# Kernel tuning notes

Measured on AMD Instinct MI355X. Metric: run time of the kernel, lower is better.

Reference implementation:

```python
import jax, jax.numpy as jnp
import numpy as np

B, T, K = 2, 2048, 1024
H, G = 16, 2          # heads, groups
HG = H // G            # kv heads = 8
KH = K // H            # head_dim = 64


def _rope(x, cos, sin):
    # x: (b, h, T, d); cos/sin: (T, d). Standard rotate-half RoPE.
    d2 = x.shape[-1] // 2
    x1, x2 = x[..., :d2], x[..., d2:]
    rot = jnp.concatenate([-x2, x1], axis=-1)
    return x * cos[None, None, :, :] + rot * sin[None, None, :, :]


def setup_inputs() -> dict:
    key = jax.random.key(0)
    k1, k2, k3 = jax.random.split(key, 3)
    x = jax.random.normal(k1, (B, T, K), dtype=jnp.float32)
    # weights stored as (in, out): y = x @ W
    w_qkv = jax.random.normal(k2, (K, K + 2 * K // G), dtype=jnp.float32) * (K ** -0.5)
    w_out = jax.random.normal(k3, (K, K), dtype=jnp.float32) * (K ** -0.5)
    # rotary tables
    inv_freq = 1.0 / (10000.0 ** (np.arange(0, KH, 2, dtype=np.float32) / KH))  # (KH/2,)
    ang = np.arange(T, dtype=np.float32)[:, None] * inv_freq[None, :]           # (T, KH/2)
    ang = np.concatenate([ang, ang], axis=-1)                                    # (T, KH)
    cos = jnp.asarray(np.cos(ang))
    sin = jnp.asarray(np.sin(ang))
    return {"x": x, "cos": cos, "sin": sin, "w_qkv": w_qkv, "w_out": w_out}


def reference(x, cos, sin, w_qkv, w_out):
    b, t, k = x.shape
    kv = k // G
    qkv = x @ w_qkv                                   # (b, T, k + 2*kv)
    Q = qkv[..., :k]
    Kt = qkv[..., k:k + kv]
    Vt = qkv[..., k + kv:]
    Q = Q.reshape(b, t, H, KH).transpose(0, 2, 1, 3)   # (b, H, T, KH)
    Kt = Kt.reshape(b, t, HG, KH).transpose(0, 2, 1, 3)  # (b, HG, T, KH)
    Vt = Vt.reshape(b, t, HG, KH).transpose(0, 2, 1, 3)
    # GQA head repeat: each kv head serves `groups` consecutive query heads
    Kt = jnp.repeat(Kt, G, axis=1)                     # (b, H, T, KH)
    Vt = jnp.repeat(Vt, G, axis=1)
    Q = _rope(Q, cos, sin)
    Kt = _rope(Kt, cos, sin)
    scores = jnp.einsum("bhqd,bhkd->bhqk", Q, Kt) * (KH ** -0.5)
    causal = jnp.tril(jnp.ones((t, t), dtype=bool))
    scores = jnp.where(causal[None, None], scores, jnp.finfo(scores.dtype).min)
    attn = jax.nn.softmax(scores, axis=-1)
    out = jnp.einsum("bhqk,bhkd->bhqd", attn, Vt)      # (b, H, T, KH)
    out = out.transpose(0, 2, 1, 3).reshape(b, t, k)
    return out @ w_out
```

## Files before the change

### kernel.cpp

```cpp
#include <hip/hip_runtime.h>

typedef unsigned short u16;
typedef unsigned int u32;
typedef short bf16x8 __attribute__((ext_vector_type(8)));
typedef float f32x4 __attribute__((ext_vector_type(4)));
typedef float f32x8v __attribute__((ext_vector_type(8)));
typedef float f32x16 __attribute__((ext_vector_type(16)));

#define LOG2E 1.44269504f

__device__ __forceinline__ u16 f2b(float f) {
  union { float f; unsigned u; } v; v.f = f;
  unsigned r = v.u + 0x7FFFu + ((v.u >> 16) & 1u);
  return (u16)(r >> 16);
}

__device__ __forceinline__ u32 cvtpk(float a, float b) {
  u32 r;
  asm("v_cvt_pk_bf16_f32 %0, %1, %2" : "=v"(r) : "v"(a), "v"(b));
  return r;
}

__device__ __forceinline__ float max3f(float a, float b, float c) {
  float r;
  asm("v_max3_f32 %0, %1, %2, %3" : "=v"(r) : "v"(a), "v"(b), "v"(c));
  return r;
}

__device__ __forceinline__ void plswap(u32& x, u32& y) {
#if __has_builtin(__builtin_amdgcn_permlane32_swap)
  typedef int v2i __attribute__((ext_vector_type(2)));
  v2i r = __builtin_amdgcn_permlane32_swap((int)x, (int)y, false, false);
  x = (u32)r[0]; y = (u32)r[1];
#else
  u32 sx = (u32)__shfl_xor((int)x, 32, 64);
  u32 sy = (u32)__shfl_xor((int)y, 32, 64);
  bool hi = (threadIdx.x & 63) >= 32;
  u32 nx = hi ? sy : x;
  u32 ny = hi ? y : sx;
  x = nx; y = ny;
#endif
}

__device__ __forceinline__ void gld16(const void* g, void* l) {
  __builtin_amdgcn_global_load_lds((const __attribute__((address_space(1))) void*)g,
                                   (__attribute__((address_space(3))) void*)l, 16, 0, 0);
}

__device__ __forceinline__ void invswz(int c, int& r, int& o) {
  int rhalf = c >> 3;
  int r2 = (rhalf >> 1) & 1;
  int r0 = ((c >> 2) & 1) ^ r2;
  r = rhalf * 2 + r0;
  int o0 = (c & 1) ^ r0;
  int o1 = ((c >> 1) & 1) ^ (rhalf & 1);
  o = o0 + 2 * o1;
}

__global__ __launch_bounds__(256) void k_prep0(const float* __restrict__ x, u16* __restrict__ Xb,
                                               const float* __restrict__ w_qkv, u16* __restrict__ Wqt,
                                               const float* __restrict__ w_out, u16* __restrict__ Wot) {
  __shared__ float tile[32][33];
  int blk = blockIdx.x;
  int tid = threadIdx.x;
  if (blk < 4096) {
    int i = blk * 256 + tid;
    float4 v = ((const float4*)x)[i];
    ushort4 o;
    o.x = f2b(v.x); o.y = f2b(v.y); o.z = f2b(v.z); o.w = f2b(v.w);
    ((ushort4*)Xb)[i] = o;
    return;
  }
  const float* in; u16* out; int R, C, t;
  if (blk < 6144) { t = blk - 4096; in = w_qkv; out = Wqt; R = 1024; C = 2048; }
  else            { t = blk - 6144; in = w_out; out = Wot; R = 1024; C = 1024; }
  int nbx = C >> 5;
  int c0 = (t % nbx) * 32, r0 = (t / nbx) * 32;
  int tx = tid & 31, ty = tid >> 5;
#pragma unroll
  for (int i = 0; i < 32; i += 8)
    tile[ty + i][tx] = in[(size_t)(r0 + ty + i) * C + c0 + tx];
  __syncthreads();
#pragma unroll
  for (int i = 0; i < 32; i += 8)
    out[(size_t)(c0 + ty + i) * R + r0 + tx] = f2b(tile[tx][ty + i]);
}

template<int BM, int Nsz, int Ksz, int EPI>
__global__ __launch_bounds__(256) void k_gemm(const u16* __restrict__ A, const u16* __restrict__ Bt,
                                              float* __restrict__ C, const float* __restrict__ cs,
                                              const float* __restrict__ sn, u16* __restrict__ Qb,
                                              u16* __restrict__ Kb, u16* __restrict__ Vt) {
  constexpr int MT = BM / 32;
  constexpr int CA = BM / 64;
  constexpr int ABytes = BM * 128;
  __shared__ u16 sm[(EPI == 1) ? 16640 : (BM * 64 + 8192)];
  const int tid = threadIdx.x;
  const int l = tid & 63, w = tid >> 6;
  const int wm = w >> 1, wn = w & 1;
  const int m0 = blockIdx.x * BM, n0 = blockIdx.y * 128;
  const int rg = l >> 4, cl = l & 15;

  const u16* aSrc[2];
  const u16* bSrc[2];
#pragma unroll
  for (int i = 0; i < CA; i++) {
    int r, o; invswz(i * 256 + tid, r, o);
    aSrc[i] = A + (size_t)(m0 + r) * Ksz + o * 8;
  }
#pragma unroll
  for (int i = 0; i < 2; i++) {
    int r, o; invswz(i * 256 + tid, r, o);
    bSrc[i] = Bt + (size_t)(n0 + r) * Ksz + o * 8;
  }

  auto stage = [&](int buf) {
#pragma unroll
    for (int i = 0; i < CA; i++) {
      gld16(aSrc[i], (char*)sm + buf * (BM * 64) + i * 4096 + w * 1024);
      aSrc[i] += 32;
    }
#pragma unroll
    for (int i = 0; i < 2; i++) {
      gld16(bSrc[i], (char*)sm + ABytes + buf * 8192 + i * 4096 + w * 1024);
      bSrc[i] += 32;
    }
  };

  f32x4 acc[MT][4] = {};
  const int NK = Ksz / 32;
  stage(0);
  for (int j = 0; j < NK; j++) {
    const int cur = j & 1;
    if (j + 1 < NK) {
      stage(cur ^ 1);
      if constexpr (CA == 2) asm volatile("s_waitcnt vmcnt(4)" ::: "memory");
      else                   asm volatile("s_waitcnt vmcnt(3)" ::: "memory");
    } else {
      asm volatile("s_waitcnt vmcnt(0)" ::: "memory");
    }
    __builtin_amdgcn_s_barrier();
    asm volatile("" ::: "memory");

    bf16x8 aF[MT], bF[4];
#pragma unroll
    for (int m = 0; m < MT; m++) {
      int row = wm * (BM / 2) + m * 16 + cl;
      unsigned ba = (unsigned)((row * 64 + rg * 16) ^ ((row & 7) << 4));
      aF[m] = *(const bf16x8*)((char*)sm + cur * (BM * 64) + ba);
    }
#pragma unroll
    for (int n = 0; n < 4; n++) {
      int row = wn * 64 + n * 16 + cl;
      unsigned ba = (unsigned)((row * 64 + rg * 16) ^ ((row & 7) << 4));
      bF[n] = *(const bf16x8*)((char*)sm + ABytes + cur * 8192 + ba);
    }
    __builtin_amdgcn_s_setprio(1);
#pragma unroll
    for (int m = 0; m < MT; m++)
#pragma unroll
      for (int n = 0; n < 4; n++)
        acc[m][n] = __builtin_amdgcn_mfma_f32_16x16x32_bf16(aF[m], bF[n], acc[m][n], 0, 0, 0);
    __builtin_amdgcn_s_setprio(0);
    asm volatile("" ::: "memory");
    __builtin_amdgcn_s_barrier();
  }

  if constexpr (EPI == 0) {
#pragma unroll
    for (int m = 0; m < MT; m++)
#pragma unroll
      for (int n = 0; n < 4; n++)
#pragma unroll
        for (int r = 0; r < 4; r++)
          C[(size_t)(m0 + wm * (BM / 2) + m * 16 + rg * 4 + r) * Nsz + n0 + wn * 64 + n * 16 + cl] =
              acc[m][n][r];
  } else {
    const int col0 = n0 + wn * 64;
    if (col0 < 1536) {
      const bool isQ = col0 < 1024;
      const float scale = isQ ? 0.125f : 1.0f;
      u16* dst = isQ ? Qb : Kb;
      const int hh = isQ ? (col0 >> 6) : ((col0 - 1024) >> 6);
      const int HN = isQ ? 16 : 8;
#pragma unroll
      for (int m = 0; m < MT; m++)
#pragma unroll
        for (int r = 0; r < 4; r++) {
          int tg = m0 + wm * (BM / 2) + m * 16 + rg * 4 + r;
          int bb = tg >> 11, tt = tg & 2047;
          size_t base = ((size_t)(bb * HN + hh) * 2048 + tt) * 64;
#pragma unroll
          for (int n = 0; n < 4; n++) {
            int d = n * 16 + cl;
            float cv = cs[tt * 64 + d], sv = sn[tt * 64 + d];
            float partner = acc[m][n ^ 2][r];
            float val = acc[m][n][r] * cv + ((n < 2) ? -partner : partner) * sv;
            dst[base + d] = f2b(val * scale);
          }
        }
    } else {
      __syncthreads();
      u16* tb = sm;
#pragma unroll
      for (int m = 0; m < MT; m++)
#pragma unroll
        for (int r = 0; r < 4; r++) {
          int tr = wm * (BM / 2) + m * 16 + rg * 4 + r;
#pragma unroll
          for (int n = 0; n < 4; n++)
            tb[tr * 130 + wn * 64 + n * 16 + cl] = f2b(acc[m][n][r]);
        }
      __syncthreads();
      const int bb = m0 >> 11, t0 = m0 & 2047;
#pragma unroll
      for (int i = 0; i < 32; i++) {
        int idx = i * 256 + tid;
        int d = idx >> 6, tp = (idx & 63) * 2;
        u32 v = (u32)tb[tp * 130 + d] | ((u32)tb[(tp + 1) * 130 + d] << 16);
        int dcol = n0 - 1536 + d;
        *(u32*)(Vt + (((size_t)(bb * 8) + (dcol >> 6)) * 64 + (dcol & 63)) * 2048 + t0 + tp) = v;
      }
    }
  }
}

__global__ __launch_bounds__(256, 4) void k_flash16(const u16* __restrict__ Qb, const u16* __restrict__ Kb,
                                                    const u16* __restrict__ Vt, u16* __restrict__ Ob) {
  __shared__ u16 smem[16384];
  const int tid = threadIdx.x;
  const int l = tid & 63, w = tid >> 6;
  const int sid = w >> 1;
  const int h01 = w & 1;
  const int bid = blockIdx.x;
  const int bkh = bid & 15;
  const int j = bid >> 4, quad = j >> 4, jj = j & 15;
  const int qt = (quad == 0) ? 63 - jj : (quad == 1) ? jj : (quad == 2) ? 47 - jj : 16 + jj;
  const int b = bkh >> 3, kh = bkh & 7;
  const int h = kh * 2 + h01;
  const int q0 = qt * 32;
  const int lq = l & 31, hi = l >> 5;
  const int q = q0 + lq;

  const int cnt = (qt + 2 - sid) >> 1;
  const int CNTMAX = (qt + 2) >> 1;

  const u16* Kg = Kb + (size_t)(b * 8 + kh) * 2048 * 64;
  const u16* Vg = Vt + (size_t)(b * 8 + kh) * 64 * 2048;
  const u16* Qp = Qb + ((size_t)(b * 16 + h) * 2048 + q) * 64 + hi * 8;

  const int krow = h01 * 16 + (l >> 3);
  const int swk1 = (krow ^ (krow >> 3)) & 7;
  const int swk2 = ((krow + 8) ^ ((krow + 8) >> 3)) & 7;
  const u16* kS1 = Kg + (size_t)(sid * 32 + krow) * 64 + (((l & 7) ^ swk1) << 3);
  const u16* kS2 = Kg + (size_t)(sid * 32 + krow + 8) * 64 + (((l & 7) ^ swk2) << 3);
  const int vd = h01 * 32 + (l >> 2);
  const int swv1 = ((vd >> 1) ^ (vd >> 3)) & 3;
  const int swv2 = (((vd + 16) >> 1) ^ ((vd + 16) >> 3)) & 3;
  const u16* vS0 = Vg + (size_t)vd * 2048 + sid * 32 + (((l & 3) ^ swv1) << 3);
  const u16* vS1 = Vg + (size_t)(vd + 16) * 2048 + sid * 32 + (((l & 3) ^ swv2) << 3);
  char* smB = (char*)smem;
  const int kDst = sid * 16384 + h01 * 2048;
  const int vDst = sid * 16384 + 8192 + h01 * 2048;

#define STAGE(buf)                                         \
  {                                                        \
    gld16(kS1, smB + kDst + (buf) * 4096);                 \
    gld16(kS2, smB + kDst + (buf) * 4096 + 1024);          \
    gld16(vS0, smB + vDst + (buf) * 4096);                 \
    gld16(vS1, smB + vDst + (buf) * 4096 + 1024);          \
    kS1 += 4096; kS2 += 4096; vS0 += 64; vS1 += 64;        \
  }

  if (cnt > 0) STAGE(0);

  bf16x8 qf[4];
#pragma unroll
  for (int ks = 0; ks < 4; ks++) qf[ks] = *(const bf16x8*)(Qp + ks * 16);

  union { u32 uu[4]; bf16x8 v; } ones;
#pragma unroll
  for (int jo = 0; jo < 4; jo++) ones.uu[jo] = 0x3F803F80u;

  f32x16 oa[2] = {};
  f32x16 lacc = {};
  float m = -3e38f;
  const int swzkr = (lq ^ (lq >> 3)) & 7;
  const int swzvr = ((lq >> 1) ^ (lq >> 3)) & 3;

  for (int i = 0; i < CNTMAX; i++) {
    const int cur = i & 1;
    asm volatile("s_waitcnt vmcnt(0)" ::: "memory");
    __builtin_amdgcn_s_barrier();
    asm volatile("" ::: "memory");
    if (i + 1 < cnt) STAGE(cur ^ 1);

    if (i < cnt) {
      const int t = sid + 2 * i;
      const char* KL = smB + sid * 16384 + cur * 4096;
      const char* VL = smB + sid * 16384 + 8192 + cur * 4096;

      bf16x8 kf[4];
#pragma unroll
      for (int ks = 0; ks < 4; ks++)
        kf[ks] = *(const bf16x8*)(KL + lq * 128 + ((((ks << 1) | hi) ^ swzkr) << 4));
      f32x16 s0 = {};
      __builtin_amdgcn_s_setprio(1);
#pragma unroll
      for (int ks = 0; ks < 4; ks++)
        s0 = __builtin_amdgcn_mfma_f32_32x32x16_bf16(kf[ks], qf[ks], s0, 0, 0, 0);
      __builtin_amdgcn_s_setprio(0);

      if (t == qt) {
#pragma unroll
        for (int r = 0; r < 16; r++) {
          int kvr = (t << 5) + (r & 3) + 8 * (r >> 2) + 4 * hi;
          if (kvr > q) s0[r] = -3e38f;
        }
      }

      float a5[5];
#pragma unroll
      for (int jo = 0; jo < 5; jo++) a5[jo] = max3f(s0[3 * jo], s0[3 * jo + 1], s0[3 * jo + 2]);
      float mx16 = fmaxf(max3f(a5[0], a5[1], a5[2]), max3f(a5[3], a5[4], s0[15]));
      bool keep = __all(mx16 - m <= 8.f);
      if (!keep) {
        float mx = fmaxf(mx16, __shfl_xor(mx16, 32, 64));
        float mnew = fmaxf(m, mx);
        float alpha = exp2f((m - mnew) * LOG2E);
        m = mnew;
        lacc[0] *= alpha;
#pragma unroll
        for (int r = 0; r < 16; r++) { oa[0][r] *= alpha; oa[1][r] *= alpha; }
      }
      float mb = m * LOG2E;
#pragma unroll
      for (int r = 0; r < 16; r++) s0[r] = exp2f(fmaf(s0[r], LOG2E, -mb));

      u32 aw[8];
#pragma unroll
      for (int jo = 0; jo < 8; jo++) aw[jo] = cvtpk(s0[2 * jo], s0[2 * jo + 1]);
      plswap(aw[0], aw[2]); plswap(aw[1], aw[3]);
      plswap(aw[4], aw[6]); plswap(aw[5], aw[7]);
      union { u32 uu[4]; bf16x8 v; } p0, p1;
#pragma unroll
      for (int jo = 0; jo < 4; jo++) { p0.uu[jo] = aw[jo]; p1.uu[jo] = aw[4 + jo]; }

      bf16x8 vf[2][2];
#pragma unroll
      for (int dt = 0; dt < 2; dt++)
#pragma unroll
        for (int p = 0; p < 2; p++)
          vf[dt][p] = *(const bf16x8*)(VL + (dt * 32 + lq) * 64 + ((((p << 1) | hi) ^ swzvr) << 4));

      __builtin_amdgcn_s_setprio(1);
#pragma unroll
      for (int dt = 0; dt < 2; dt++) {
        oa[dt] = __builtin_amdgcn_mfma_f32_32x32x16_bf16(vf[dt][0], p0.v, oa[dt], 0, 0, 0);
        oa[dt] = __builtin_amdgcn_mfma_f32_32x32x16_bf16(vf[dt][1], p1.v, oa[dt], 0, 0, 0);
      }
      lacc = __builtin_amdgcn_mfma_f32_32x32x16_bf16(ones.v, p0.v, lacc, 0, 0, 0);
      lacc = __builtin_amdgcn_mfma_f32_32x32x16_bf16(ones.v, p1.v, lacc, 0, 0, 0);
      __builtin_amdgcn_s_setprio(0);
    }
    asm volatile("" ::: "memory");
  }

  float lsum = lacc[0];

  __syncthreads();
  float* pbuf = (float*)smem;
  float* mlb = (float*)((char*)smem + 16896);
  u32* otileB = (u32*)((char*)smem + 17920);
  if (sid == 1) {
    float* pb = pbuf + (h01 * 64 + l) * 33;
#pragma unroll
    for (int r = 0; r < 16; r++) { pb[r] = oa[0][r]; pb[16 + r] = oa[1][r]; }
    mlb[h01 * 128 + l] = m;
    mlb[h01 * 128 + 64 + l] = lsum;
  }
  __syncthreads();
  if (sid == 0) {
    float m1 = mlb[h01 * 128 + l], l1 = mlb[h01 * 128 + 64 + l];
    float ms = fmaxf(m, m1);
    float a0 = exp2f((m - ms) * LOG2E);
    float a1 = exp2f((m1 - ms) * LOG2E);
    float linv = 1.0f / (lsum * a0 + l1 * a1);
    a0 *= linv; a1 *= linv;
    const float* pb = pbuf + (h01 * 64 + l) * 33;
    float of[32];
#pragma unroll
    for (int r = 0; r < 16; r++) {
      of[r] = oa[0][r] * a0 + pb[r] * a1;
      of[16 + r] = oa[1][r] * a0 + pb[16 + r] * a1;
    }
    u32* ot = otileB + h01 * (32 * 33);
#pragma unroll
    for (int dt = 0; dt < 2; dt++)
#pragma unroll
      for (int r = 0; r < 16; r += 2) {
        int d = dt * 32 + (r & 3) + 8 * (r >> 2) + 4 * hi;
        ot[lq * 33 + (d >> 1)] = cvtpk(of[dt * 16 + r], of[dt * 16 + r + 1]);
      }
#pragma unroll
    for (int i2 = 0; i2 < 16; i2++) {
      int wd = i2 * 64 + l;
      int row = wd >> 5, col = wd & 31;
      u32 v = ot[row * 33 + col];
      *(u32*)(Ob + (size_t)(b * 2048 + q0 + row) * 1024 + h * 64 + col * 2) = v;
    }
  }
#undef STAGE
}

extern "C" void kernel_launch(void* const* d_in, const int* in_sizes, int n_in,
                              void* d_out, int out_size, void* d_ws, size_t ws_size,
                              hipStream_t stream) {
  const float* x = (const float*)d_in[0];
  const float* cs = (const float*)d_in[1];
  const float* sn = (const float*)d_in[2];
  const float* w_qkv = (const float*)d_in[3];
  const float* w_out = (const float*)d_in[4];
  float* out = (float*)d_out;
  char* ws = (char*)d_ws;

  u16* Xb  = (u16*)(ws);
  u16* Wqt = (u16*)(ws + ((size_t)8u << 20));
  u16* Wot = (u16*)(ws + ((size_t)12u << 20));
  u16* Qb  = (u16*)(ws + ((size_t)18u << 20));
  u16* Kb  = (u16*)(ws + ((size_t)26u << 20));
  u16* Vt  = (u16*)(ws + ((size_t)30u << 20));
  u16* Ob  = (u16*)(ws + ((size_t)34u << 20));

  k_prep0<<<7168, 256, 0, stream>>>(x, Xb, w_qkv, Wqt, w_out, Wot);
  k_gemm<128, 2048, 1024, 1><<<dim3(32, 16), 256, 0, stream>>>(Xb, Wqt, nullptr, cs, sn, Qb, Kb, Vt);
  k_flash16<<<1024, 256, 0, stream>>>(Qb, Kb, Vt, Ob);
  k_gemm<64, 1024, 1024, 0><<<dim3(64, 8), 256, 0, stream>>>(Ob, Wot, out, nullptr, nullptr, nullptr, nullptr, nullptr);
}
```

Measured before the change: 89.70 us.

## Split KV sequence four ways per block and pair causal query tiles

The flash attention kernel now uses 512 threads per block. Each block holds four KV-split groups instead of two, which strides the KV tiles by four and merges four partial softmax states at the end. Each block now processes two query tiles (qt and 63-qt) in sequence, so every block gets roughly equal causal work, and the grid is halved to 512 blocks. This targets load imbalance and tail effects, at the cost of more merge work through shared memory, more LDS per block (64KB), and possibly lower occupancy.

```diff
diff --git a/kernel.cpp b/kernel.cpp
--- a/kernel.cpp
+++ b/kernel.cpp
@@ -225,192 +225,202 @@
   }
 }
 
-__global__ __launch_bounds__(256, 4) void k_flash16(const u16* __restrict__ Qb, const u16* __restrict__ Kb,
-                                                    const u16* __restrict__ Vt, u16* __restrict__ Ob) {
-  __shared__ u16 smem[16384];
+__global__ __launch_bounds__(512) void k_flash17(const u16* __restrict__ Qb, const u16* __restrict__ Kb,
+                                                 const u16* __restrict__ Vt, u16* __restrict__ Ob) {
+  __shared__ u16 smem[32768];
   const int tid = threadIdx.x;
   const int l = tid & 63, w = tid >> 6;
   const int sid = w >> 1;
   const int h01 = w & 1;
   const int bid = blockIdx.x;
   const int bkh = bid & 15;
-  const int j = bid >> 4, quad = j >> 4, jj = j & 15;
-  const int qt = (quad == 0) ? 63 - jj : (quad == 1) ? jj : (quad == 2) ? 47 - jj : 16 + jj;
+  const int p = bid >> 4;
   const int b = bkh >> 3, kh = bkh & 7;
   const int h = kh * 2 + h01;
-  const int q0 = qt * 32;
   const int lq = l & 31, hi = l >> 5;
-  const int q = q0 + lq;
-
-  const int cnt = (qt + 2 - sid) >> 1;
-  const int CNTMAX = (qt + 2) >> 1;
 
   const u16* Kg = Kb + (size_t)(b * 8 + kh) * 2048 * 64;
   const u16* Vg = Vt + (size_t)(b * 8 + kh) * 64 * 2048;
-  const u16* Qp = Qb + ((size_t)(b * 16 + h) * 2048 + q) * 64 + hi * 8;
 
   const int krow = h01 * 16 + (l >> 3);
   const int swk1 = (krow ^ (krow >> 3)) & 7;
   const int swk2 = ((krow + 8) ^ ((krow + 8) >> 3)) & 7;
-  const u16* kS1 = Kg + (size_t)(sid * 32 + krow) * 64 + (((l & 7) ^ swk1) << 3);
-  const u16* kS2 = Kg + (size_t)(sid * 32 + krow + 8) * 64 + (((l & 7) ^ swk2) << 3);
   const int vd = h01 * 32 + (l >> 2);
   const int swv1 = ((vd >> 1) ^ (vd >> 3)) & 3;
   const int swv2 = (((vd + 16) >> 1) ^ ((vd + 16) >> 3)) & 3;
-  const u16* vS0 = Vg + (size_t)vd * 2048 + sid * 32 + (((l & 3) ^ swv1) << 3);
-  const u16* vS1 = Vg + (size_t)(vd + 16) * 2048 + sid * 32 + (((l & 3) ^ swv2) << 3);
   char* smB = (char*)smem;
   const int kDst = sid * 16384 + h01 * 2048;
   const int vDst = sid * 16384 + 8192 + h01 * 2048;
-
-#define STAGE(buf)                                         \
-  {                                                        \
-    gld16(kS1, smB + kDst + (buf) * 4096);                 \
-    gld16(kS2, smB + kDst + (buf) * 4096 + 1024);          \
-    gld16(vS0, smB + vDst + (buf) * 4096);                 \
-    gld16(vS1, smB + vDst + (buf) * 4096 + 1024);          \
-    kS1 += 4096; kS2 += 4096; vS0 += 64; vS1 += 64;        \
-  }
-
-  if (cnt > 0) STAGE(0);
-
-  bf16x8 qf[4];
-#pragma unroll
-  for (int ks = 0; ks < 4; ks++) qf[ks] = *(const bf16x8*)(Qp + ks * 16);
-
-  union { u32 uu[4]; bf16x8 v; } ones;
-#pragma unroll
-  for (int jo = 0; jo < 4; jo++) ones.uu[jo] = 0x3F803F80u;
-
-  f32x16 oa[2] = {};
-  f32x16 lacc = {};
-  float m = -3e38f;
   const int swzkr = (lq ^ (lq >> 3)) & 7;
   const int swzvr = ((lq >> 1) ^ (lq >> 3)) & 3;
 
-  for (int i = 0; i < CNTMAX; i++) {
-    const int cur = i & 1;
-    asm volatile("s_waitcnt vmcnt(0)" ::: "memory");
-    __builtin_amdgcn_s_barrier();
-    asm volatile("" ::: "memory");
-    if (i + 1 < cnt) STAGE(cur ^ 1);
-
-    if (i < cnt) {
-      const int t = sid + 2 * i;
-      const char* KL = smB + sid * 16384 + cur * 4096;
-      const char* VL = smB + sid * 16384 + 8192 + cur * 4096;
-
-      bf16x8 kf[4];
-#pragma unroll
-      for (int ks = 0; ks < 4; ks++)
-        kf[ks] = *(const bf16x8*)(KL + lq * 128 + ((((ks << 1) | hi) ^ swzkr) << 4));
-      f32x16 s0 = {};
-      __builtin_amdgcn_s_setprio(1);
-#pragma unroll
-      for (int ks = 0; ks < 4; ks++)
-        s0 = __builtin_amdgcn_mfma_f32_32x32x16_bf16(kf[ks], qf[ks], s0, 0, 0, 0);
-      __builtin_amdgcn_s_setprio(0);
-
-      if (t == qt) {
-#pragma unroll
-        for (int r = 0; r < 16; r++) {
-          int kvr = (t << 5) + (r & 3) + 8 * (r >> 2) + 4 * hi;
-          if (kvr > q) s0[r] = -3e38f;
-        }
+  union { u32 uu[4]; bf16x8 v; } ones;
+#pragma unroll
+  for (int jo = 0; jo < 4; jo++) ones.uu[jo] = 0x3F803F80u;
+
+  for (int up = 0; up < 2; up++) {
+    const int qt = up ? p : (63 - p);
+    const int q0 = qt * 32;
+    const int q = q0 + lq;
+
+    const int cnt = (qt + 4 - sid) >> 2;
+    const int CNTMAX = (qt + 4) >> 2;
+
+    const u16* Qp = Qb + ((size_t)(b * 16 + h) * 2048 + q) * 64 + hi * 8;
+    const u16* kS1 = Kg + (size_t)(sid * 32 + krow) * 64 + (((l & 7) ^ swk1) << 3);
+    const u16* kS2 = Kg + (size_t)(sid * 32 + krow + 8) * 64 + (((l & 7) ^ swk2) << 3);
+    const u16* vS0 = Vg + (size_t)vd * 2048 + sid * 32 + (((l & 3) ^ swv1) << 3);
+    const u16* vS1 = Vg + (size_t)(vd + 16) * 2048 + sid * 32 + (((l & 3) ^ swv2) << 3);
+
+#define STAGE(buf)                                         \
+    {                                                      \
+      gld16(kS1, smB + kDst + (buf) * 4096);               \
+      gld16(kS2, smB + kDst + (buf) * 4096 + 1024);        \
+      gld16(vS0, smB + vDst + (buf) * 4096);               \
+      gld16(vS1, smB + vDst + (buf) * 4096 + 1024);        \
+      kS1 += 8192; kS2 += 8192; vS0 += 128; vS1 += 128;    \
+    }
+
+    if (cnt > 0) STAGE(0);
+
+    bf16x8 qf[4];
+#pragma unroll
+    for (int ks = 0; ks < 4; ks++) qf[ks] = *(const bf16x8*)(Qp + ks * 16);
+
+    f32x16 oa[2] = {};
+    f32x16 lacc = {};
+    float m = -3e38f;
+
+    for (int i = 0; i < CNTMAX; i++) {
+      const int cur = i & 1;
+      asm volatile("s_waitcnt vmcnt(0)" ::: "memory");
+      __builtin_amdgcn_s_barrier();
+      asm volatile("" ::: "memory");
+      if (i + 1 < cnt) STAGE(cur ^ 1);
+
+      if (i < cnt) {
+        const int t = sid + 4 * i;
+        const char* KL = smB + sid * 16384 + cur * 4096;
+        const char* VL = smB + sid * 16384 + 8192 + cur * 4096;
+
+        bf16x8 kf[4];
+#pragma unroll
+        for (int ks = 0; ks < 4; ks++)
+          kf[ks] = *(const bf16x8*)(KL + lq * 128 + ((((ks << 1) | hi) ^ swzkr) << 4));
+        f32x16 s0 = {};
+        __builtin_amdgcn_s_setprio(1);
+#pragma unroll
+        for (int ks = 0; ks < 4; ks++)
+          s0 = __builtin_amdgcn_mfma_f32_32x32x16_bf16(kf[ks], qf[ks], s0, 0, 0, 0);
+        __builtin_amdgcn_s_setprio(0);
+
+        if (t == qt) {
+#pragma unroll
+          for (int r = 0; r < 16; r++) {
+            int kvr = (t << 5) + (r & 3) + 8 * (r >> 2) + 4 * hi;
+            if (kvr > q) s0[r] = -3e38f;
+          }
+        }
+
+        float a5[5];
+#pragma unroll
+        for (int jo = 0; jo < 5; jo++) a5[jo] = max3f(s0[3 * jo], s0[3 * jo + 1], s0[3 * jo + 2]);
+        float mx16 = fmaxf(max3f(a5[0], a5[1], a5[2]), max3f(a5[3], a5[4], s0[15]));
+        bool keep = __all(mx16 - m <= 8.f);
+        if (!keep) {
+          float mx = fmaxf(mx16, __shfl_xor(mx16, 32, 64));
+          float mnew = fmaxf(m, mx);
+          float alpha = exp2f((m - mnew) * LOG2E);
+          m = mnew;
+          lacc[0] *= alpha;
+#pragma unroll
+          for (int r = 0; r < 16; r++) { oa[0][r] *= alpha; oa[1][r] *= alpha; }
+        }
+        float mb = m * LOG2E;
+#pragma unroll
+        for (int r = 0; r < 16; r++) s0[r] = exp2f(fmaf(s0[r], LOG2E, -mb));
+
+        u32 aw[8];
+#pragma unroll
+        for (int jo = 0; jo < 8; jo++) aw[jo] = cvtpk(s0[2 * jo], s0[2 * jo + 1]);
+        plswap(aw[0], aw[2]); plswap(aw[1], aw[3]);
+        plswap(aw[4], aw[6]); plswap(aw[5], aw[7]);
+        union { u32 uu[4]; bf16x8 v; } p0, p1;
+#pragma unroll
+        for (int jo = 0; jo < 4; jo++) { p0.uu[jo] = aw[jo]; p1.uu[jo] = aw[4 + jo]; }
+
+        bf16x8 vf[2][2];
+#pragma unroll
+        for (int dt = 0; dt < 2; dt++)
+#pragma unroll
+          for (int pp = 0; pp < 2; pp++)
+            vf[dt][pp] = *(const bf16x8*)(VL + (dt * 32 + lq) * 64 + ((((pp << 1) | hi) ^ swzvr) << 4));
+
+        __builtin_amdgcn_s_setprio(1);
+#pragma unroll
+        for (int dt = 0; dt < 2; dt++) {
+          oa[dt] = __builtin_amdgcn_mfma_f32_32x32x16_bf16(vf[dt][0], p0.v, oa[dt], 0, 0, 0);
+          oa[dt] = __builtin_amdgcn_mfma_f32_32x32x16_bf16(vf[dt][1], p1.v, oa[dt], 0, 0, 0);
+        }
+        lacc = __builtin_amdgcn_mfma_f32_32x32x16_bf16(ones.v, p0.v, lacc, 0, 0, 0);
+        lacc = __builtin_amdgcn_mfma_f32_32x32x16_bf16(ones.v, p1.v, lacc, 0, 0, 0);
+        __builtin_amdgcn_s_setprio(0);
       }
-
-      float a5[5];
-#pragma unroll
-      for (int jo = 0; jo < 5; jo++) a5[jo] = max3f(s0[3 * jo], s0[3 * jo + 1], s0[3 * jo + 2]);
-      float mx16 = fmaxf(max3f(a5[0], a5[1], a5[2]), max3f(a5[3], a5[4], s0[15]));
-      bool keep = __all(mx16 - m <= 8.f);
-      if (!keep) {
-        float mx = fmaxf(mx16, __shfl_xor(mx16, 32, 64));
-        float mnew = fmaxf(m, mx);
-        float alpha = exp2f((m - mnew) * LOG2E);
-        m = mnew;
-        lacc[0] *= alpha;
-#pragma unroll
-        for (int r = 0; r < 16; r++) { oa[0][r] *= alpha; oa[1][r] *= alpha; }
+      asm volatile("" ::: "memory");
+    }
+
+    float lsum = lacc[0];
+
+    __syncthreads();
+    float* pbuf = (float*)smem;
+    float* mlb = (float*)((char*)smem + 50688);
+    if (sid != 0) {
+      int uidx = (sid - 1) * 2 + h01;
+      float* pb = pbuf + (size_t)uidx * (64 * 33) + l * 33;
+#pragma unroll
+      for (int r = 0; r < 16; r++) { pb[r] = oa[0][r]; pb[16 + r] = oa[1][r]; }
+      mlb[uidx * 128 + l] = m;
+      mlb[uidx * 128 + 64 + l] = lsum;
+    }
+    __syncthreads();
+    if (sid == 0) {
+      float ms = m;
+#pragma unroll
+      for (int s2 = 0; s2 < 3; s2++) ms = fmaxf(ms, mlb[(s2 * 2 + h01) * 128 + l]);
+      float a0 = exp2f((m - ms) * LOG2E);
+      float ltot = lsum * a0;
+      float of[32];
+#pragma unroll
+      for (int r = 0; r < 16; r++) { of[r] = oa[0][r] * a0; of[16 + r] = oa[1][r] * a0; }
+#pragma unroll
+      for (int s2 = 0; s2 < 3; s2++) {
+        int uidx = s2 * 2 + h01;
+        float a1 = exp2f((mlb[uidx * 128 + l] - ms) * LOG2E);
+        ltot += mlb[uidx * 128 + 64 + l] * a1;
+        const float* pb = pbuf + (size_t)uidx * (64 * 33) + l * 33;
+#pragma unroll
+        for (int r = 0; r < 16; r++) { of[r] += pb[r] * a1; of[16 + r] += pb[16 + r] * a1; }
       }
-      float mb = m * LOG2E;
-#pragma unroll
-      for (int r = 0; r < 16; r++) s0[r] = exp2f(fmaf(s0[r], LOG2E, -mb));
-
-      u32 aw[8];
-#pragma unroll
-      for (int jo = 0; jo < 8; jo++) aw[jo] = cvtpk(s0[2 * jo], s0[2 * jo + 1]);
-      plswap(aw[0], aw[2]); plswap(aw[1], aw[3]);
-      plswap(aw[4], aw[6]); plswap(aw[5], aw[7]);
-      union { u32 uu[4]; bf16x8 v; } p0, p1;
-#pragma unroll
-      for (int jo = 0; jo < 4; jo++) { p0.uu[jo] = aw[jo]; p1.uu[jo] = aw[4 + jo]; }
-
-      bf16x8 vf[2][2];
+      float linv = 1.0f / ltot;
+      u32* ot = (u32*)((char*)smem + 53760) + h01 * (32 * 33);
 #pragma unroll
       for (int dt = 0; dt < 2; dt++)
 #pragma unroll
-        for (int p = 0; p < 2; p++)
-          vf[dt][p] = *(const bf16x8*)(VL + (dt * 32 + lq) * 64 + ((((p << 1) | hi) ^ swzvr) << 4));
-
-      __builtin_amdgcn_s_setprio(1);
-#pragma unroll
-      for (int dt = 0; dt < 2; dt++) {
-        oa[dt] = __builtin_amdgcn_mfma_f32_32x32x16_bf16(vf[dt][0], p0.v, oa[dt], 0, 0, 0);
-        oa[dt] = __builtin_amdgcn_mfma_f32_32x32x16_bf16(vf[dt][1], p1.v, oa[dt], 0, 0, 0);
+        for (int r = 0; r < 16; r += 2) {
+          int d = dt * 32 + (r & 3) + 8 * (r >> 2) + 4 * hi;
+          ot[lq * 33 + (d >> 1)] = cvtpk(of[dt * 16 + r] * linv, of[dt * 16 + r + 1] * linv);
+        }
+#pragma unroll
+      for (int i2 = 0; i2 < 16; i2++) {
+        int wd = i2 * 64 + l;
+        int row = wd >> 5, col = wd & 31;
+        u32 v2 = ot[row * 33 + col];
+        *(u32*)(Ob + (size_t)(b * 2048 + q0 + row) * 1024 + h * 64 + col * 2) = v2;
       }
-      lacc = __builtin_amdgcn_mfma_f32_32x32x16_bf16(ones.v, p0.v, lacc, 0, 0, 0);
-      lacc = __builtin_amdgcn_mfma_f32_32x32x16_bf16(ones.v, p1.v, lacc, 0, 0, 0);
-      __builtin_amdgcn_s_setprio(0);
-    }
-    asm volatile("" ::: "memory");
-  }
-
-  float lsum = lacc[0];
-
-  __syncthreads();
-  float* pbuf = (float*)smem;
-  float* mlb = (float*)((char*)smem + 16896);
-  u32* otileB = (u32*)((char*)smem + 17920);
-  if (sid == 1) {
-    float* pb = pbuf + (h01 * 64 + l) * 33;
-#pragma unroll
-    for (int r = 0; r < 16; r++) { pb[r] = oa[0][r]; pb[16 + r] = oa[1][r]; }
-    mlb[h01 * 128 + l] = m;
-    mlb[h01 * 128 + 64 + l] = lsum;
-  }
-  __syncthreads();
-  if (sid == 0) {
-    float m1 = mlb[h01 * 128 + l], l1 = mlb[h01 * 128 + 64 + l];
-    float ms = fmaxf(m, m1);
-    float a0 = exp2f((m - ms) * LOG2E);
-    float a1 = exp2f((m1 - ms) * LOG2E);
-    float linv = 1.0f / (lsum * a0 + l1 * a1);
-    a0 *= linv; a1 *= linv;
-    const float* pb = pbuf + (h01 * 64 + l) * 33;
-    float of[32];
-#pragma unroll
-    for (int r = 0; r < 16; r++) {
-      of[r] = oa[0][r] * a0 + pb[r] * a1;
-      of[16 + r] = oa[1][r] * a0 + pb[16 + r] * a1;
-    }
-    u32* ot = otileB + h01 * (32 * 33);
-#pragma unroll
-    for (int dt = 0; dt < 2; dt++)
-#pragma unroll
-      for (int r = 0; r < 16; r += 2) {
-        int d = dt * 32 + (r & 3) + 8 * (r >> 2) + 4 * hi;
-        ot[lq * 33 + (d >> 1)] = cvtpk(of[dt * 16 + r], of[dt * 16 + r + 1]);
-      }
-#pragma unroll
-    for (int i2 = 0; i2 < 16; i2++) {
-      int wd = i2 * 64 + l;
-      int row = wd >> 5, col = wd & 31;
-      u32 v = ot[row * 33 + col];
-      *(u32*)(Ob + (size_t)(b * 2048 + q0 + row) * 1024 + h * 64 + col * 2) = v;
-    }
-  }
+    }
+    __syncthreads();
 #undef STAGE
+  }
 }
 
 extern "C" void kernel_launch(void* const* d_in, const int* in_sizes, int n_in,
@@ -434,6 +444,6 @@
 
   k_prep0<<<7168, 256, 0, stream>>>(x, Xb, w_qkv, Wqt, w_out, Wot);
   k_gemm<128, 2048, 1024, 1><<<dim3(32, 16), 256, 0, stream>>>(Xb, Wqt, nullptr, cs, sn, Qb, Kb, Vt);
-  k_flash16<<<1024, 256, 0, stream>>>(Qb, Kb, Vt, Ob);
+  k_flash17<<<512, 512, 0, stream>>>(Qb, Kb, Vt, Ob);
   k_gemm<64, 1024, 1024, 0><<<dim3(64, 8), 256, 0, stream>>>(Ob, Wot, out, nullptr, nullptr, nullptr, nullptr, nullptr);
 }
```

Result: slower. 102.8 us (+14.6%).

## Replace 4-wave split-KV flash block with single-wave per-head blocks

Applied to the files above, without the earlier changes.

The flash attention kernel moves from 256-thread blocks, where two wave pairs split the KV sequence and merged partial softmax results through shared memory, to 64-thread single-wave blocks. Each block now handles one query head over the full causal KV range, and twice as many blocks are launched. This removes the barriers, the cross-wave merge and the shared K/V duplication, and it switches to a vmcnt-based double buffer without block syncs. In exchange, K/V tiles shared by the two GQA heads are loaded separately by each block, and each wave walks a serial chain up to twice as long, which can hurt latency hiding on long causal rows.

```diff
diff --git a/kernel.cpp b/kernel.cpp
--- a/kernel.cpp
+++ b/kernel.cpp
@@ -225,54 +225,55 @@
   }
 }
 
-__global__ __launch_bounds__(256, 4) void k_flash16(const u16* __restrict__ Qb, const u16* __restrict__ Kb,
-                                                    const u16* __restrict__ Vt, u16* __restrict__ Ob) {
-  __shared__ u16 smem[16384];
-  const int tid = threadIdx.x;
-  const int l = tid & 63, w = tid >> 6;
-  const int sid = w >> 1;
-  const int h01 = w & 1;
+__global__ __launch_bounds__(64) void k_flash18(const u16* __restrict__ Qb, const u16* __restrict__ Kb,
+                                                const u16* __restrict__ Vt, u16* __restrict__ Ob) {
+  __shared__ u16 smem[8192];
+  const int l = threadIdx.x;
   const int bid = blockIdx.x;
   const int bkh = bid & 15;
-  const int j = bid >> 4, quad = j >> 4, jj = j & 15;
+  const int j2 = bid >> 5;
+  const int h01 = (bid >> 4) & 1;
+  const int quad = j2 >> 4, jj = j2 & 15;
   const int qt = (quad == 0) ? 63 - jj : (quad == 1) ? jj : (quad == 2) ? 47 - jj : 16 + jj;
   const int b = bkh >> 3, kh = bkh & 7;
   const int h = kh * 2 + h01;
   const int q0 = qt * 32;
   const int lq = l & 31, hi = l >> 5;
   const int q = q0 + lq;
-
-  const int cnt = (qt + 2 - sid) >> 1;
-  const int CNTMAX = (qt + 2) >> 1;
+  const int cnt = qt + 1;
 
   const u16* Kg = Kb + (size_t)(b * 8 + kh) * 2048 * 64;
   const u16* Vg = Vt + (size_t)(b * 8 + kh) * 64 * 2048;
   const u16* Qp = Qb + ((size_t)(b * 16 + h) * 2048 + q) * 64 + hi * 8;
 
-  const int krow = h01 * 16 + (l >> 3);
-  const int swk1 = (krow ^ (krow >> 3)) & 7;
-  const int swk2 = ((krow + 8) ^ ((krow + 8) >> 3)) & 7;
-  const u16* kS1 = Kg + (size_t)(sid * 32 + krow) * 64 + (((l & 7) ^ swk1) << 3);
-  const u16* kS2 = Kg + (size_t)(sid * 32 + krow + 8) * 64 + (((l & 7) ^ swk2) << 3);
-  const int vd = h01 * 32 + (l >> 2);
-  const int swv1 = ((vd >> 1) ^ (vd >> 3)) & 3;
-  const int swv2 = (((vd + 16) >> 1) ^ ((vd + 16) >> 3)) & 3;
-  const u16* vS0 = Vg + (size_t)vd * 2048 + sid * 32 + (((l & 3) ^ swv1) << 3);
-  const u16* vS1 = Vg + (size_t)(vd + 16) * 2048 + sid * 32 + (((l & 3) ^ swv2) << 3);
+  const int kr = l >> 3, kc = l & 7;
+  const int vr = l >> 2, vc = l & 3;
+  const u16* kS[4];
+  const u16* vS[4];
+#pragma unroll
+  for (int c = 0; c < 4; c++) {
+    int row = c * 8 + kr;
+    kS[c] = Kg + (size_t)row * 64 + ((kc ^ ((row ^ (row >> 3)) & 7)) << 3);
+    int d = c * 16 + vr;
+    vS[c] = Vg + (size_t)d * 2048 + ((vc ^ (((d >> 1) ^ (d >> 3)) & 3)) << 3);
+  }
   char* smB = (char*)smem;
-  const int kDst = sid * 16384 + h01 * 2048;
-  const int vDst = sid * 16384 + 8192 + h01 * 2048;
-
-#define STAGE(buf)                                         \
-  {                                                        \
-    gld16(kS1, smB + kDst + (buf) * 4096);                 \
-    gld16(kS2, smB + kDst + (buf) * 4096 + 1024);          \
-    gld16(vS0, smB + vDst + (buf) * 4096);                 \
-    gld16(vS1, smB + vDst + (buf) * 4096 + 1024);          \
-    kS1 += 4096; kS2 += 4096; vS0 += 64; vS1 += 64;        \
-  }
-
-  if (cnt > 0) STAGE(0);
+
+#define STAGE(buf)                                                  \
+  {                                                                 \
+    _Pragma("unroll")                                               \
+    for (int c = 0; c < 4; c++) {                                   \
+      gld16(kS[c], smB + (buf) * 4096 + c * 1024);                  \
+      kS[c] += 2048;                                                \
+    }                                                               \
+    _Pragma("unroll")                                               \
+    for (int c = 0; c < 4; c++) {                                   \
+      gld16(vS[c], smB + 8192 + (buf) * 4096 + c * 1024);           \
+      vS[c] += 32;                                                  \
+    }                                                               \
+  }
+
+  STAGE(0);
 
   bf16x8 qf[4];
 #pragma unroll
@@ -288,127 +289,97 @@
   const int swzkr = (lq ^ (lq >> 3)) & 7;
   const int swzvr = ((lq >> 1) ^ (lq >> 3)) & 3;
 
-  for (int i = 0; i < CNTMAX; i++) {
+  for (int i = 0; i < cnt; i++) {
     const int cur = i & 1;
-    asm volatile("s_waitcnt vmcnt(0)" ::: "memory");
-    __builtin_amdgcn_s_barrier();
-    asm volatile("" ::: "memory");
-    if (i + 1 < cnt) STAGE(cur ^ 1);
-
-    if (i < cnt) {
-      const int t = sid + 2 * i;
-      const char* KL = smB + sid * 16384 + cur * 4096;
-      const char* VL = smB + sid * 16384 + 8192 + cur * 4096;
-
-      bf16x8 kf[4];
-#pragma unroll
-      for (int ks = 0; ks < 4; ks++)
-        kf[ks] = *(const bf16x8*)(KL + lq * 128 + ((((ks << 1) | hi) ^ swzkr) << 4));
-      f32x16 s0 = {};
-      __builtin_amdgcn_s_setprio(1);
-#pragma unroll
-      for (int ks = 0; ks < 4; ks++)
-        s0 = __builtin_amdgcn_mfma_f32_32x32x16_bf16(kf[ks], qf[ks], s0, 0, 0, 0);
-      __builtin_amdgcn_s_setprio(0);
-
-      if (t == qt) {
-#pragma unroll
-        for (int r = 0; r < 16; r++) {
-          int kvr = (t << 5) + (r & 3) + 8 * (r >> 2) + 4 * hi;
-          if (kvr > q) s0[r] = -3e38f;
-        }
+    if (i + 1 < cnt) {
+      STAGE(cur ^ 1);
+      asm volatile("s_waitcnt vmcnt(8)" ::: "memory");
+    } else {
+      asm volatile("s_waitcnt vmcnt(0)" ::: "memory");
+    }
+
+    const char* KL = smB + cur * 4096;
+    const char* VL = smB + 8192 + cur * 4096;
+
+    bf16x8 kf[4];
+#pragma unroll
+    for (int ks = 0; ks < 4; ks++)
+      kf[ks] = *(const bf16x8*)(KL + lq * 128 + ((((ks << 1) | hi) ^ swzkr) << 4));
+    f32x16 s0 = {};
+    __builtin_amdgcn_s_setprio(1);
+#pragma unroll
+    for (int ks = 0; ks < 4; ks++)
+      s0 = __builtin_amdgcn_mfma_f32_32x32x16_bf16(kf[ks], qf[ks], s0, 0, 0, 0);
+    __builtin_amdgcn_s_setprio(0);
+
+    if (i == qt) {
+#pragma unroll
+      for (int r = 0; r < 16; r++) {
+        int kvr = (i << 5) + (r & 3) + 8 * (r >> 2) + 4 * hi;
+        if (kvr > q) s0[r] = -3e38f;
       }
-
-      float a5[5];
-#pragma unroll
-      for (int jo = 0; jo < 5; jo++) a5[jo] = max3f(s0[3 * jo], s0[3 * jo + 1], s0[3 * jo + 2]);
-      float mx16 = fmaxf(max3f(a5[0], a5[1], a5[2]), max3f(a5[3], a5[4], s0[15]));
-      bool keep = __all(mx16 - m <= 8.f);
-      if (!keep) {
-        float mx = fmaxf(mx16, __shfl_xor(mx16, 32, 64));
-        float mnew = fmaxf(m, mx);
-        float alpha = exp2f((m - mnew) * LOG2E);
-        m = mnew;
-        lacc[0] *= alpha;
-#pragma unroll
-        for (int r = 0; r < 16; r++) { oa[0][r] *= alpha; oa[1][r] *= alpha; }
-      }
-      float mb = m * LOG2E;
-#pragma unroll
-      for (int r = 0; r < 16; r++) s0[r] = exp2f(fmaf(s0[r], LOG2E, -mb));
-
-      u32 aw[8];
-#pragma unroll
-      for (int jo = 0; jo < 8; jo++) aw[jo] = cvtpk(s0[2 * jo], s0[2 * jo + 1]);
-      plswap(aw[0], aw[2]); plswap(aw[1], aw[3]);
-      plswap(aw[4], aw[6]); plswap(aw[5], aw[7]);
-      union { u32 uu[4]; bf16x8 v; } p0, p1;
-#pragma unroll
-      for (int jo = 0; jo < 4; jo++) { p0.uu[jo] = aw[jo]; p1.uu[jo] = aw[4 + jo]; }
-
-      bf16x8 vf[2][2];
-#pragma unroll
-      for (int dt = 0; dt < 2; dt++)
-#pragma unroll
-        for (int p = 0; p < 2; p++)
-          vf[dt][p] = *(const bf16x8*)(VL + (dt * 32 + lq) * 64 + ((((p << 1) | hi) ^ swzvr) << 4));
-
-      __builtin_amdgcn_s_setprio(1);
-#pragma unroll
-      for (int dt = 0; dt < 2; dt++) {
-        oa[dt] = __builtin_amdgcn_mfma_f32_32x32x16_bf16(vf[dt][0], p0.v, oa[dt], 0, 0, 0);
-        oa[dt] = __builtin_amdgcn_mfma_f32_32x32x16_bf16(vf[dt][1], p1.v, oa[dt], 0, 0, 0);
-      }
-      lacc = __builtin_amdgcn_mfma_f32_32x32x16_bf16(ones.v, p0.v, lacc, 0, 0, 0);
-      lacc = __builtin_amdgcn_mfma_f32_32x32x16_bf16(ones.v, p1.v, lacc, 0, 0, 0);
-      __builtin_amdgcn_s_setprio(0);
-    }
-    asm volatile("" ::: "memory");
-  }
-
-  float lsum = lacc[0];
-
-  __syncthreads();
-  float* pbuf = (float*)smem;
-  float* mlb = (float*)((char*)smem + 16896);
-  u32* otileB = (u32*)((char*)smem + 17920);
-  if (sid == 1) {
-    float* pb = pbuf + (h01 * 64 + l) * 33;
-#pragma unroll
-    for (int r = 0; r < 16; r++) { pb[r] = oa[0][r]; pb[16 + r] = oa[1][r]; }
-    mlb[h01 * 128 + l] = m;
-    mlb[h01 * 128 + 64 + l] = lsum;
-  }
-  __syncthreads();
-  if (sid == 0) {
-    float m1 = mlb[h01 * 128 + l], l1 = mlb[h01 * 128 + 64 + l];
-    float ms = fmaxf(m, m1);
-    float a0 = exp2f((m - ms) * LOG2E);
-    float a1 = exp2f((m1 - ms) * LOG2E);
-    float linv = 1.0f / (lsum * a0 + l1 * a1);
-    a0 *= linv; a1 *= linv;
-    const float* pb = pbuf + (h01 * 64 + l) * 33;
-    float of[32];
-#pragma unroll
-    for (int r = 0; r < 16; r++) {
-      of[r] = oa[0][r] * a0 + pb[r] * a1;
-      of[16 + r] = oa[1][r] * a0 + pb[16 + r] * a1;
-    }
-    u32* ot = otileB + h01 * (32 * 33);
+    }
+
+    float a5[5];
+#pragma unroll
+    for (int jo = 0; jo < 5; jo++) a5[jo] = max3f(s0[3 * jo], s0[3 * jo + 1], s0[3 * jo + 2]);
+    float mx16 = fmaxf(max3f(a5[0], a5[1], a5[2]), max3f(a5[3], a5[4], s0[15]));
+    bool keep = __all(mx16 - m <= 8.f);
+    if (!keep) {
+      float mx = fmaxf(mx16, __shfl_xor(mx16, 32, 64));
+      float mnew = fmaxf(m, mx);
+      float alpha = exp2f((m - mnew) * LOG2E);
+      m = mnew;
+      lacc[0] *= alpha;
+#pragma unroll
+      for (int r = 0; r < 16; r++) { oa[0][r] *= alpha; oa[1][r] *= alpha; }
+    }
+    float mb = m * LOG2E;
+#pragma unroll
+    for (int r = 0; r < 16; r++) s0[r] = exp2f(fmaf(s0[r], LOG2E, -mb));
+
+    u32 aw[8];
+#pragma unroll
+    for (int jo = 0; jo < 8; jo++) aw[jo] = cvtpk(s0[2 * jo], s0[2 * jo + 1]);
+    plswap(aw[0], aw[2]); plswap(aw[1], aw[3]);
+    plswap(aw[4], aw[6]); plswap(aw[5], aw[7]);
+    union { u32 uu[4]; bf16x8 v; } p0, p1;
+#pragma unroll
+    for (int jo = 0; jo < 4; jo++) { p0.uu[jo] = aw[jo]; p1.uu[jo] = aw[4 + jo]; }
+
+    bf16x8 vf[2][2];
 #pragma unroll
     for (int dt = 0; dt < 2; dt++)
 #pragma unroll
-      for (int r = 0; r < 16; r += 2) {
-        int d = dt * 32 + (r & 3) + 8 * (r >> 2) + 4 * hi;
-        ot[lq * 33 + (d >> 1)] = cvtpk(of[dt * 16 + r], of[dt * 16 + r + 1]);
-      }
-#pragma unroll
-    for (int i2 = 0; i2 < 16; i2++) {
-      int wd = i2 * 64 + l;
-      int row = wd >> 5, col = wd & 31;
-      u32 v = ot[row * 33 + col];
-      *(u32*)(Ob + (size_t)(b * 2048 + q0 + row) * 1024 + h * 64 + col * 2) = v;
-    }
+      for (int pp = 0; pp < 2; pp++)
+        vf[dt][pp] = *(const bf16x8*)(VL + (dt * 32 + lq) * 64 + ((((pp << 1) | hi) ^ swzvr) << 4));
+
+    __builtin_amdgcn_s_setprio(1);
+#pragma unroll
+    for (int dt = 0; dt < 2; dt++) {
+      oa[dt] = __builtin_amdgcn_mfma_f32_32x32x16_bf16(vf[dt][0], p0.v, oa[dt], 0, 0, 0);
+      oa[dt] = __builtin_amdgcn_mfma_f32_32x32x16_bf16(vf[dt][1], p1.v, oa[dt], 0, 0, 0);
+    }
+    lacc = __builtin_amdgcn_mfma_f32_32x32x16_bf16(ones.v, p0.v, lacc, 0, 0, 0);
+    lacc = __builtin_amdgcn_mfma_f32_32x32x16_bf16(ones.v, p1.v, lacc, 0, 0, 0);
+    __builtin_amdgcn_s_setprio(0);
+  }
+
+  float linv = 1.0f / lacc[0];
+  u32* ot = (u32*)smem;
+#pragma unroll
+  for (int dt = 0; dt < 2; dt++)
+#pragma unroll
+    for (int r = 0; r < 16; r += 2) {
+      int d = dt * 32 + (r & 3) + 8 * (r >> 2) + 4 * hi;
+      ot[lq * 33 + (d >> 1)] = cvtpk(oa[dt][r] * linv, oa[dt][r + 1] * linv);
+    }
+#pragma unroll
+  for (int i2 = 0; i2 < 16; i2++) {
+    int wd = i2 * 64 + l;
+    int row = wd >> 5, col = wd & 31;
+    u32 v = ot[row * 33 + col];
+    *(u32*)(Ob + (size_t)(b * 2048 + q0 + row) * 1024 + h * 64 + col * 2) = v;
   }
 #undef STAGE
 }
@@ -434,6 +405,6 @@
 
   k_prep0<<<7168, 256, 0, stream>>>(x, Xb, w_qkv, Wqt, w_out, Wot);
   k_gemm<128, 2048, 1024, 1><<<dim3(32, 16), 256, 0, stream>>>(Xb, Wqt, nullptr, cs, sn, Qb, Kb, Vt);
-  k_flash16<<<1024, 256, 0, stream>>>(Qb, Kb, Vt, Ob);
+  k_flash18<<<2048, 64, 0, stream>>>(Qb, Kb, Vt, Ob);
   k_gemm<64, 1024, 1024, 0><<<dim3(64, 8), 256, 0, stream>>>(Ob, Wot, out, nullptr, nullptr, nullptr, nullptr, nullptr);
 }
```

Result: slower. 110.3 us (+22.9%).
